# Kernel tuning notes

Hardware: AMD Instinct MI355X
Metric: run time of the kernel (lower is better)

## Reference

```python
import jax, jax.numpy as jnp
import numpy as np

IN_CHANNELS = 512
NUM_HEADS = 8
PARTIAL = 4
PC = IN_CHANNELS // PARTIAL  # 128, per-branch dim


def _mha(x, wqkv, bqkv, wproj, bproj, num_heads):
    # Standard ViT-style attention block: fused qkv -> SDPA -> out proj.
    B, N, C = x.shape
    d = C // num_heads
    qkv = (x @ wqkv + bqkv).reshape(B, N, 3, num_heads, d)
    q, k, v = jnp.moveaxis(qkv, 2, 0)            # each (B, N, h, d)
    q = q.transpose(0, 2, 1, 3)                  # (B, h, N, d)
    k = k.transpose(0, 2, 1, 3)
    v = v.transpose(0, 2, 1, 3)
    scale = jnp.asarray(d, x.dtype) ** -0.5
    attn = jax.nn.softmax(jnp.einsum('bhqd,bhkd->bhqk', q, k) * scale, axis=-1)
    out = jnp.einsum('bhqk,bhkd->bhqd', attn, v)
    out = out.transpose(0, 2, 1, 3).reshape(B, N, C)
    return out @ wproj + bproj


def _channel_shuffle(x, groups):
    # ShuffleNet channel shuffle on (b, c, n, t)
    b, c, n, t = x.shape
    return x.reshape(b, groups, c // groups, n, t).transpose(0, 2, 1, 3, 4).reshape(b, c, n, t)


def setup_inputs() -> dict:
    key = jax.random.key(0)
    ks = jax.random.split(key, 13)
    b, n, t = 8, 25, 64
    inp = {'x': jax.random.normal(ks[0], (b, n, t, IN_CHANNELS), dtype=jnp.float32)}
    i = 1
    for name in ('t', 's', 'st'):
        inp[f'{name}_wqkv'] = jax.random.normal(ks[i], (PC, 3 * PC), dtype=jnp.float32) * 0.02; i += 1
        inp[f'{name}_bqkv'] = jnp.zeros((3 * PC,), dtype=jnp.float32)
        inp[f'{name}_wproj'] = jax.random.normal(ks[i], (PC, PC), dtype=jnp.float32) * 0.02; i += 1
        inp[f'{name}_bproj'] = jnp.zeros((PC,), dtype=jnp.float32)
    return inp


def reference(x, t_wqkv, t_bqkv, t_wproj, t_bproj,
              s_wqkv, s_bqkv, s_wproj, s_bproj,
              st_wqkv, st_bqkv, st_wproj, st_bproj):
    b, n, t, c = x.shape
    pc = PC
    # split order in forward: x_id, x_st, x_s, x_t (all width pc here)
    x_id = x[..., 0 * pc:1 * pc]
    x_st = x[..., 1 * pc:2 * pc]
    x_s = x[..., 2 * pc:3 * pc]
    x_t = x[..., 3 * pc:4 * pc]

    t_x = x_t.reshape(b * n, t, pc)                       # temporal: attend over t
    s_x = x_s.transpose(0, 2, 1, 3).reshape(b * t, n, pc)  # spatial: attend over n
    st_x = x_st.reshape(b, n * t, pc)                      # spatiotemporal: attend over n*t

    t_x = _mha(t_x, t_wqkv, t_bqkv, t_wproj, t_bproj, NUM_HEADS).reshape(b, n, t, pc)
    s_x = _mha(s_x, s_wqkv, s_bqkv, s_wproj, s_bproj, NUM_HEADS).reshape(b, t, n, pc).transpose(0, 2, 1, 3)
    st_x = _mha(st_x, st_wqkv, st_bqkv, st_wproj, st_bproj, NUM_HEADS).reshape(b, n, t, pc)

    # concat order: id, t, s, st (differs from split order), then to channels-first
    out = jnp.concatenate((x_id, t_x, s_x, st_x), axis=3).transpose(0, 3, 1, 2)  # (b, c, n, t)
    return _channel_shuffle(out, PARTIAL)
```

## Files before the change

### kernel.cpp

```cpp
#include <hip/hip_runtime.h>
#include <hip/hip_bf16.h>

#define BUF   1638400ull
#define QSC   0.36067376f

typedef __attribute__((ext_vector_type(4))) float f4;
typedef __attribute__((ext_vector_type(8))) short s8v;
typedef __attribute__((ext_vector_type(4))) unsigned u4v;

#if __has_builtin(__builtin_amdgcn_exp2f)
#define EXP2(x) __builtin_amdgcn_exp2f(x)
#else
#define EXP2(x) exp2f(x)
#endif

__device__ __forceinline__ short f2bf(float f) {
    __hip_bfloat16 h = __float2bfloat16(f);
    short s; __builtin_memcpy(&s, &h, 2); return s;
}
__device__ __forceinline__ unsigned pack2(float a, float b) {
    return (unsigned)(unsigned short)f2bf(a) | ((unsigned)(unsigned short)f2bf(b) << 16);
}
__device__ __forceinline__ float bf2f(short s) {
    return __uint_as_float((unsigned)(unsigned short)s << 16);
}
__device__ __forceinline__ unsigned tpack(float hi, float lo) {
    return __builtin_amdgcn_perm(__float_as_uint(hi), __float_as_uint(lo), 0x07060302u);
}

__global__ __launch_bounds__(256) void prep(
    const float* __restrict__ x,
    const float* __restrict__ wq0, const float* __restrict__ wq1,
    const float* __restrict__ wq2,
    const float* __restrict__ wp0, const float* __restrict__ wp1,
    const float* __restrict__ wp2,
    short* __restrict__ xbf, short* __restrict__ wsw)
{
    const int blk = blockIdx.x, tid = threadIdx.x;
    if (blk < 3200) {
        const int base = blk * 2048 + tid * 8;
        float4 a = *(const float4*)(x + base);
        float4 b = *(const float4*)(x + base + 4);
        s8v o;
        o[0]=f2bf(a.x); o[1]=f2bf(a.y); o[2]=f2bf(a.z); o[3]=f2bf(a.w);
        o[4]=f2bf(b.x); o[5]=f2bf(b.y); o[6]=f2bf(b.z); o[7]=f2bf(b.w);
        *(s8v*)(xbf + base) = o;
    } else {
        const int idx0 = (blk - 3200) * 2048 + tid * 8;
        const float* W; int Ncols, loc = idx0;
        if      (idx0 < 49152)  { W = wq0; Ncols = 384; }
        else if (idx0 < 98304)  { W = wq1; Ncols = 384; loc -= 49152; }
        else if (idx0 < 147456) { W = wq2; Ncols = 384; loc -= 98304; }
        else if (idx0 < 163840) { W = wp0; Ncols = 128; loc -= 147456; }
        else if (idx0 < 180224) { W = wp1; Ncols = 128; loc -= 163840; }
        else                    { W = wp2; Ncols = 128; loc -= 180224; }
        const int lane = (loc >> 3) & 63, ks = (loc >> 9) & 3, nt = loc >> 11;
        const int col = nt * 16 + (lane & 15);
        const int k0  = ks * 32 + 8 * (lane >> 4);
        s8v o;
#pragma unroll
        for (int j = 0; j < 8; j++) o[j] = f2bf(W[(k0 + j) * Ncols + col]);
        *(s8v*)(wsw + idx0) = o;
    }
}

__global__ __launch_bounds__(256) void qkv_all(
    const short* __restrict__ xbf, const short* __restrict__ wsw,
    const float* __restrict__ bq0, const float* __restrict__ bq1,
    const float* __restrict__ bq2,
    short* __restrict__ q0, short* __restrict__ k0, short* __restrict__ vt0,
    short* __restrict__ q1, short* __restrict__ k1, short* __restrict__ vt1,
    short* __restrict__ q2, short* __restrict__ k2, short* __restrict__ vt2)
{
    const int br = blockIdx.x / 800, tile = blockIdx.x % 800;
    const int tok0 = tile * 16;
    const int wave = threadIdx.x >> 6, lane = threadIdx.x & 63;
    const int c = lane & 15, gq = lane >> 4;
    const int off = 384 - 128 * br;
    const short* wswb = wsw + br * 49152;
    const float* bias = (br == 0) ? bq0 : (br == 1) ? bq1 : bq2;

    const short* xrow = xbf + (size_t)(tok0 + c) * 512 + off + 8 * gq;
    s8v af[4];
#pragma unroll
    for (int ks = 0; ks < 4; ks++) af[ks] = *(const s8v*)(xrow + ks * 32);

    const int batch0 = tok0 >> 6;
    const int b_  = tok0 / 1600;
    const int rm0 = tok0 - b_ * 1600;
    const int seq1 = rm0 >> 6;

    for (int nti = 0; nti < 6; nti++) {
        const int nt = wave * 6 + nti;
        const short* bp = wswb + ((size_t)(nt * 4) * 64 + lane) * 8;
        f4 acc = {0.f, 0.f, 0.f, 0.f};
#pragma unroll
        for (int ks = 0; ks < 4; ks++) {
            s8v bf = *(const s8v*)(bp + ks * 512);
            acc = __builtin_amdgcn_mfma_f32_16x16x32_bf16(af[ks], bf, acc, 0, 0, 0);
        }
        const float bv = bias[nt * 16 + c];
        const float v0 = acc[0]+bv, v1 = acc[1]+bv, v2 = acc[2]+bv, v3 = acc[3]+bv;
        const int which = nt >> 3, h = nt & 7;

        if (br == 0) {
            const int seq0 = (tok0 & 63) + 4 * gq;
            if (which == 2) {
                unsigned* p = (unsigned*)(vt0 + ((size_t)(batch0*8+h)*16 + c)*64 + seq0);
                p[0] = pack2(v0, v1); p[1] = pack2(v2, v3);
            } else {
                short* p = (which ? k0 : q0) + (((size_t)(batch0*8+h)*64 + seq0)*16 + c);
                p[0]=f2bf(v0); p[16]=f2bf(v1); p[32]=f2bf(v2); p[48]=f2bf(v3);
            }
        } else if (br == 1) {
            const int bt0 = b_ * 64 + (rm0 & 63) + 4 * gq;
            if (which == 2) {
                short* p = vt1 + ((size_t)(bt0*8+h)*16 + c)*25 + seq1;
                p[0]=f2bf(v0); p[3200]=f2bf(v1); p[6400]=f2bf(v2); p[9600]=f2bf(v3);
            } else {
                short* p = (which ? k1 : q1) + (((size_t)bt0*8+h)*25 + seq1)*16 + c;
                p[0]=f2bf(v0); p[3200]=f2bf(v1); p[6400]=f2bf(v2); p[9600]=f2bf(v3);
            }
        } else {
            const int seq0 = rm0 + 4 * gq;
            if (which == 2) {
                unsigned* p = (unsigned*)(vt2 + ((size_t)b_*128 + h*16 + c)*1600 + seq0);
                p[0] = pack2(v0, v1); p[1] = pack2(v2, v3);
            } else {
                short* p = (which ? k2 : q2) + (((size_t)b_*8+h)*1600 + seq0)*16 + c;
                p[0]=f2bf(v0); p[16]=f2bf(v1); p[32]=f2bf(v2); p[48]=f2bf(v3);
            }
        }
    }
}

template<int CHK, int NCH, bool KM>
__device__ __forceinline__ void attn_core(
    const short* __restrict__ qg, const short* __restrict__ kg,
    const short* __restrict__ vtg, const int vstride, const int nreal,
    short* kl, short* vt, const int stid, const int snum,
    const int lane, const int qt0, const int nq,
    float* __restrict__ obase, const int ostride)
{
    const int c = lane & 15, gq = lane >> 4;
    const int VS = CHK + 8;

    u4v qu = {0u, 0u, 0u, 0u};
    if (gq < 2) {
        const int qrow = KM ? min(qt0 + c, nq - 1) : (qt0 + c);
        const short* qr = qg + (size_t)qrow * 16 + 8 * gq;
        s8v raw = *(const s8v*)qr;
#pragma unroll
        for (int jp = 0; jp < 4; jp++)
            qu[jp] = tpack(bf2f(raw[2*jp+1]) * QSC, bf2f(raw[2*jp]) * QSC);
    }
    const s8v qf = __builtin_bit_cast(s8v, qu);

    s8v ones;
#pragma unroll
    for (int j = 0; j < 8; j++) ones[j] = (short)0x3F80;

    f4 oacc = {0.f,0.f,0.f,0.f}, lacc = {0.f,0.f,0.f,0.f};
    const int krow_base = 8 * (c >> 2) + (c & 3);

    for (int ch = 0; ch < NCH; ch++) {
        const int kb0 = ch * CHK;
        __syncthreads();
        if (KM) {
            for (int i = stid; i < CHK * 16 + 8; i += snum)
                kl[i] = (i < nreal * 16) ? kg[i] : (short)0;
            for (int i = stid; i < 16 * VS; i += snum) {
                int d = i / VS, col = i % VS;
                vt[i] = (col < nreal) ? vtg[(size_t)d * vstride + col] : (short)0;
            }
        } else {
            const unsigned* kgd = (const unsigned*)(kg + (size_t)kb0 * 16);
            unsigned* kld = (unsigned*)kl;
            for (int i = stid; i < CHK * 8 + 4; i += snum)
                kld[i] = (i < CHK * 8) ? kgd[i] : 0u;
            for (int i = stid; i < 16 * (CHK / 2); i += snum) {
                int d = i / (CHK / 2), cc = i % (CHK / 2);
                *(unsigned*)(vt + d * VS + 2 * cc) =
                    *(const unsigned*)(vtg + (size_t)d * vstride + kb0 + 2 * cc);
            }
        }
        __syncthreads();

#pragma unroll
        for (int st = 0; st < CHK / 32; st++) {
            const int kr0 = st * 32 + krow_base;
            s8v kf0 = *(const s8v*)(gq < 2 ? kl + kr0 * 16 + 8 * gq       : kl + CHK * 16);
            s8v kf1 = *(const s8v*)(gq < 2 ? kl + (kr0 + 4) * 16 + 8 * gq : kl + CHK * 16);
            s8v vf  = *(const s8v*)(vt + c * VS + st * 32 + 8 * gq);

            const f4 z = {0.f,0.f,0.f,0.f};
            f4 sa = __builtin_amdgcn_mfma_f32_16x16x32_bf16(kf0, qf, z, 0, 0, 0);
            f4 sb = __builtin_amdgcn_mfma_f32_16x16x32_bf16(kf1, qf, z, 0, 0, 0);

            float pa[4], pb[4];
#pragma unroll
            for (int r = 0; r < 4; r++) { pa[r] = EXP2(sa[r]); pb[r] = EXP2(sb[r]); }
            if (KM) {
#pragma unroll
                for (int r = 0; r < 4; r++) {
                    if (kb0 + st*32 + 8*gq + r     >= nreal) pa[r] = 0.f;
                    if (kb0 + st*32 + 8*gq + 4 + r >= nreal) pb[r] = 0.f;
                }
            }
            u4v pu;
            pu[0] = tpack(pa[1], pa[0]); pu[1] = tpack(pa[3], pa[2]);
            pu[2] = tpack(pb[1], pb[0]); pu[3] = tpack(pb[3], pb[2]);
            s8v pf = __builtin_bit_cast(s8v, pu);

            oacc = __builtin_amdgcn_mfma_f32_16x16x32_bf16(pf, vf,   oacc, 0, 0, 0);
            lacc = __builtin_amdgcn_mfma_f32_16x16x32_bf16(pf, ones, lacc, 0, 0, 0);
        }
    }

#pragma unroll
    for (int r = 0; r < 4; r++) {
        const int qrow = qt0 + 4 * gq + r;
        if (!KM || qrow < nq)
            obase[(size_t)qrow * ostride] = oacc[r] / lacc[r];
    }
}

__global__ __launch_bounds__(256) void attn_all(
    const short* __restrict__ q0, const short* __restrict__ k0, const short* __restrict__ vt0,
    const short* __restrict__ q1, const short* __restrict__ k1, const short* __restrict__ vt1,
    const short* __restrict__ q2, const short* __restrict__ k2, const short* __restrict__ vt2,
    float* __restrict__ ob0, float* __restrict__ ob1, float* __restrict__ ob2)
{
    __shared__ short smem[5264];
    const int blk = blockIdx.x, tid = threadIdx.x;
    const int wave = tid >> 6, lane = tid & 63;
    const int c = lane & 15;

    if (blk < 1600) {
        const int bh = blk / 25, b25 = blk % 25;
        const int qt0 = b25 * 64 + wave * 16;
        float* obase = ob2 + (size_t)(bh >> 3) * 1600 * 128 + (bh & 7) * 16 + c;
        attn_core<160, 10, false>(q2 + (size_t)bh * 25600, k2 + (size_t)bh * 25600,
                                  vt2 + (size_t)bh * 25600, 1600, 1600,
                                  smem, smem + 2568, tid, 256,
                                  lane, qt0, 1600, obase, 128);
    } else if (blk < 3200) {
        const int bh = blk - 1600;
        float* obase = ob0 + (size_t)(bh >> 3) * 64 * 128 + (bh & 7) * 16 + c;
        attn_core<64, 1, false>(q0 + (size_t)bh * 1024, k0 + (size_t)bh * 1024,
                                vt0 + (size_t)bh * 1024, 64, 64,
                                smem, smem + 1040, tid, 256,
                                lane, wave * 16, 64, obase, 128);
    } else {
        const int bs = blk - 3200;
        const int half = wave >> 1;
        const int bh = bs * 2 + half;
        const int qt0 = (wave & 1) * 16;
        short* kl = smem + half * 1160;
        const int bat = bh >> 3, h = bh & 7;
        const int b2 = bat >> 6, t2 = bat & 63;
        float* obase = ob1 + ((size_t)b2 * 1600 + t2) * 128 + h * 16 + c;
        attn_core<32, 1, true>(q1 + (size_t)bh * 400, k1 + (size_t)bh * 400,
                               vt1 + (size_t)bh * 400, 25, 25,
                               kl, kl + 520, tid & 127, 128,
                               lane, qt0, 25, obase, 8192);
    }
}

__global__ __launch_bounds__(256) void projid(
    const float* __restrict__ ob0, const float* __restrict__ ob1,
    const float* __restrict__ ob2, const short* __restrict__ wsw,
    const float* __restrict__ bp0, const float* __restrict__ bp1,
    const float* __restrict__ bp2,
    const float* __restrict__ x, float* __restrict__ out)
{
    __shared__ unsigned short xl[64 * 130];
    const int blk = blockIdx.x, tid = threadIdx.x;

    if (blk < 2400) {
        const int br = blk / 800, t8 = blk % 800;
        const float* obb = (br == 0) ? ob0 : (br == 1) ? ob1 : ob2;
        const float* bp  = (br == 0) ? bp0 : (br == 1) ? bp1 : bp2;
        const short* wswb = wsw + 147456 + br * 16384;
        const int grp = br + 1;
        const int tok0 = t8 * 16;
        const int wave = tid >> 6, lane = tid & 63;
        const int c = lane & 15, gq = lane >> 4;

        const float* arow = obb + (size_t)(tok0 + c) * 128 + 8 * gq;
        s8v af[4];
#pragma unroll
        for (int ks = 0; ks < 4; ks++) {
            float4 a = *(const float4*)(arow + ks * 32);
            float4 b = *(const float4*)(arow + ks * 32 + 4);
            af[ks][0]=f2bf(a.x); af[ks][1]=f2bf(a.y); af[ks][2]=f2bf(a.z); af[ks][3]=f2bf(a.w);
            af[ks][4]=f2bf(b.x); af[ks][5]=f2bf(b.y); af[ks][6]=f2bf(b.z); af[ks][7]=f2bf(b.w);
        }

        const int bn = t8 >> 2, b_ = bn / 25, n_ = bn % 25;
        const int t0 = (t8 & 3) * 16 + 4 * gq;

        for (int nti = 0; nti < 2; nti++) {
            const int nt = wave * 2 + nti;
            const short* bpw = wswb + ((size_t)(nt * 4) * 64 + lane) * 8;
            f4 acc = {0.f, 0.f, 0.f, 0.f};
#pragma unroll
            for (int ks = 0; ks < 4; ks++) {
                s8v bf = *(const s8v*)(bpw + ks * 512);
                acc = __builtin_amdgcn_mfma_f32_16x16x32_bf16(af[ks], bf, acc, 0, 0, 0);
            }
            const int c2 = nt * 16 + c;
            const float bv = bp[c2];
            float4 st = {acc[0]+bv, acc[1]+bv, acc[2]+bv, acc[3]+bv};
            *(float4*)(out + (size_t)b_ * 819200 + (size_t)(c2 * 4 + grp) * 1600
                           + n_ * 64 + t0) = st;
        }
    } else {
        const int bn = blk - 2400;
        const int b_ = bn / 25, n_ = bn % 25;
        for (int idx = tid; idx < 8192; idx += 256) {
            int row = idx >> 7, c2 = idx & 127;
            xl[row * 130 + c2] =
                (unsigned short)(__float_as_uint(x[(size_t)(bn * 64 + row) * 512 + c2]) >> 16);
        }
        __syncthreads();
        const int t_ = tid & 63, cg = tid >> 6;
        const size_t base = (size_t)b_ * 819200 + (size_t)n_ * 64 + t_;
#pragma unroll
        for (int i = 0; i < 32; i++) {
            int c2 = cg + 4 * i;
            out[base + (size_t)(c2 * 4 + 0) * 1600] =
                __uint_as_float((unsigned)xl[t_ * 130 + c2] << 16);
        }
    }
}

extern "C" void kernel_launch(void* const* d_in, const int* in_sizes, int n_in,
                              void* d_out, int out_size, void* d_ws, size_t ws_size,
                              hipStream_t stream)
{
    const float* x        = (const float*)d_in[0];
    const float* t_wqkv   = (const float*)d_in[1];
    const float* t_bqkv   = (const float*)d_in[2];
    const float* t_wproj  = (const float*)d_in[3];
    const float* t_bproj  = (const float*)d_in[4];
    const float* s_wqkv   = (const float*)d_in[5];
    const float* s_bqkv   = (const float*)d_in[6];
    const float* s_wproj  = (const float*)d_in[7];
    const float* s_bproj  = (const float*)d_in[8];
    const float* st_wqkv  = (const float*)d_in[9];
    const float* st_bqkv  = (const float*)d_in[10];
    const float* st_wproj = (const float*)d_in[11];
    const float* st_bproj = (const float*)d_in[12];

    short* xbf = (short*)d_ws;
    short* wsw = xbf + 6553600ull;
    short* qkv = wsw + 196608ull;
    short *q0 = qkv,           *k0 = qkv + BUF,     *vt0 = qkv + 2*BUF;
    short *q1 = qkv + 3*BUF,   *k1 = qkv + 4*BUF,   *vt1 = qkv + 5*BUF;
    short *q2 = qkv + 6*BUF,   *k2 = qkv + 7*BUF,   *vt2 = qkv + 8*BUF;
    float* ob0 = (float*)(qkv + 9*BUF);
    float* ob1 = ob0 + BUF;
    float* ob2 = ob0 + 2*BUF;
    float* out = (float*)d_out;

    prep<<<3296, 256, 0, stream>>>(x, t_wqkv, s_wqkv, st_wqkv,
                                   t_wproj, s_wproj, st_wproj, xbf, wsw);
    qkv_all<<<2400, 256, 0, stream>>>(xbf, wsw, t_bqkv, s_bqkv, st_bqkv,
                                      q0, k0, vt0, q1, k1, vt1, q2, k2, vt2);
    attn_all<<<5248, 256, 0, stream>>>(q0, k0, vt0, q1, k1, vt1, q2, k2, vt2,
                                       ob0, ob1, ob2);
    projid<<<2600, 256, 0, stream>>>(ob0, ob1, ob2, wsw,
                                     t_bproj, s_bproj, st_bproj, x, out);
}
```

Baseline: 189.1 us.

## Rewrite attention with 32x32 MFMA, drop x bf16 prep pass, bf16 attention outputs

Removes the separate pass that converted x to bf16; the qkv kernel now reads fp32 x and packs it to bf16 inline. Attention moves from the LDS-staged 16x16 MFMA scheme to a per-wave 32x32x16 MFMA kernel that reads K/V directly from global memory with no shared memory or barriers. The softmax denominator comes from a row of ones in a global buffer fused into the PV MFMA and is read back with a lane shuffle. The spatial V buffer is padded to 32 and the attention outputs are written as bf16, which halves traffic into the projection kernel. The trade-offs are uncached global K/V loads and extra rounding of the intermediate outputs.

```diff
diff --git a/kernel.cpp b/kernel.cpp
--- a/kernel.cpp
+++ b/kernel.cpp
@@ -4,15 +4,21 @@
 #define BUF   1638400ull
 #define QSC   0.36067376f
 
-typedef __attribute__((ext_vector_type(4))) float f4;
-typedef __attribute__((ext_vector_type(8))) short s8v;
-typedef __attribute__((ext_vector_type(4))) unsigned u4v;
+typedef __attribute__((ext_vector_type(4)))  float    f4;
+typedef __attribute__((ext_vector_type(16))) float    f16v;
+typedef __attribute__((ext_vector_type(8)))  short    s8v;
+typedef __attribute__((ext_vector_type(4)))  unsigned u4v;
 
 #if __has_builtin(__builtin_amdgcn_exp2f)
 #define EXP2(x) __builtin_amdgcn_exp2f(x)
 #else
 #define EXP2(x) exp2f(x)
 #endif
+#if __has_builtin(__builtin_amdgcn_rcpf)
+#define RCP(x) __builtin_amdgcn_rcpf(x)
+#else
+#define RCP(x) (1.0f/(x))
+#endif
 
 __device__ __forceinline__ short f2bf(float f) {
     __hip_bfloat16 h = __float2bfloat16(f);
@@ -27,26 +33,23 @@
 __device__ __forceinline__ unsigned tpack(float hi, float lo) {
     return __builtin_amdgcn_perm(__float_as_uint(hi), __float_as_uint(lo), 0x07060302u);
 }
+__device__ __forceinline__ f16v zf16() {
+    f16v z;
+#pragma unroll
+    for (int i = 0; i < 16; i++) z[i] = 0.f;
+    return z;
+}
 
 __global__ __launch_bounds__(256) void prep(
-    const float* __restrict__ x,
     const float* __restrict__ wq0, const float* __restrict__ wq1,
     const float* __restrict__ wq2,
     const float* __restrict__ wp0, const float* __restrict__ wp1,
     const float* __restrict__ wp2,
-    short* __restrict__ xbf, short* __restrict__ wsw)
+    short* __restrict__ wsw, short* __restrict__ onesb)
 {
     const int blk = blockIdx.x, tid = threadIdx.x;
-    if (blk < 3200) {
-        const int base = blk * 2048 + tid * 8;
-        float4 a = *(const float4*)(x + base);
-        float4 b = *(const float4*)(x + base + 4);
-        s8v o;
-        o[0]=f2bf(a.x); o[1]=f2bf(a.y); o[2]=f2bf(a.z); o[3]=f2bf(a.w);
-        o[4]=f2bf(b.x); o[5]=f2bf(b.y); o[6]=f2bf(b.z); o[7]=f2bf(b.w);
-        *(s8v*)(xbf + base) = o;
-    } else {
-        const int idx0 = (blk - 3200) * 2048 + tid * 8;
+    if (blk < 96) {
+        const int idx0 = blk * 2048 + tid * 8;
         const float* W; int Ncols, loc = idx0;
         if      (idx0 < 49152)  { W = wq0; Ncols = 384; }
         else if (idx0 < 98304)  { W = wq1; Ncols = 384; loc -= 49152; }
@@ -61,11 +64,16 @@
 #pragma unroll
         for (int j = 0; j < 8; j++) o[j] = f2bf(W[(k0 + j) * Ncols + col]);
         *(s8v*)(wsw + idx0) = o;
+    } else {
+        s8v o;
+#pragma unroll
+        for (int j = 0; j < 8; j++) o[j] = (short)0x3F80;
+        *(s8v*)(onesb + tid * 8) = o;
     }
 }
 
 __global__ __launch_bounds__(256) void qkv_all(
-    const short* __restrict__ xbf, const short* __restrict__ wsw,
+    const float* __restrict__ x, const short* __restrict__ wsw,
     const float* __restrict__ bq0, const float* __restrict__ bq1,
     const float* __restrict__ bq2,
     short* __restrict__ q0, short* __restrict__ k0, short* __restrict__ vt0,
@@ -80,10 +88,17 @@
     const short* wswb = wsw + br * 49152;
     const float* bias = (br == 0) ? bq0 : (br == 1) ? bq1 : bq2;
 
-    const short* xrow = xbf + (size_t)(tok0 + c) * 512 + off + 8 * gq;
+    const float* xrow = x + (size_t)(tok0 + c) * 512 + off + 8 * gq;
     s8v af[4];
 #pragma unroll
-    for (int ks = 0; ks < 4; ks++) af[ks] = *(const s8v*)(xrow + ks * 32);
+    for (int ks = 0; ks < 4; ks++) {
+        float4 a = *(const float4*)(xrow + ks * 32);
+        float4 b = *(const float4*)(xrow + ks * 32 + 4);
+        u4v t;
+        t[0] = tpack(a.y, a.x); t[1] = tpack(a.w, a.z);
+        t[2] = tpack(b.y, b.x); t[3] = tpack(b.w, b.z);
+        af[ks] = __builtin_bit_cast(s8v, t);
+    }
 
     const int batch0 = tok0 >> 6;
     const int b_  = tok0 / 1600;
@@ -115,8 +130,8 @@
         } else if (br == 1) {
             const int bt0 = b_ * 64 + (rm0 & 63) + 4 * gq;
             if (which == 2) {
-                short* p = vt1 + ((size_t)(bt0*8+h)*16 + c)*25 + seq1;
-                p[0]=f2bf(v0); p[3200]=f2bf(v1); p[6400]=f2bf(v2); p[9600]=f2bf(v3);
+                short* p = vt1 + ((size_t)(bt0*8+h)*16 + c)*32 + seq1;
+                p[0]=f2bf(v0); p[4096]=f2bf(v1); p[8192]=f2bf(v2); p[12288]=f2bf(v3);
             } else {
                 short* p = (which ? k1 : q1) + (((size_t)bt0*8+h)*25 + seq1)*16 + c;
                 p[0]=f2bf(v0); p[3200]=f2bf(v1); p[6400]=f2bf(v2); p[9600]=f2bf(v3);
@@ -134,94 +149,63 @@
     }
 }
 
-template<int CHK, int NCH, bool KM>
-__device__ __forceinline__ void attn_core(
+template<int NSTEPS, bool MASK>
+__device__ __forceinline__ void attn32(
     const short* __restrict__ qg, const short* __restrict__ kg,
-    const short* __restrict__ vtg, const int vstride, const int nreal,
-    short* kl, short* vt, const int stid, const int snum,
-    const int lane, const int qt0, const int nq,
-    float* __restrict__ obase, const int ostride)
-{
-    const int c = lane & 15, gq = lane >> 4;
-    const int VS = CHK + 8;
-
-    u4v qu = {0u, 0u, 0u, 0u};
-    if (gq < 2) {
-        const int qrow = KM ? min(qt0 + c, nq - 1) : (qt0 + c);
-        const short* qr = qg + (size_t)qrow * 16 + 8 * gq;
-        s8v raw = *(const s8v*)qr;
-#pragma unroll
-        for (int jp = 0; jp < 4; jp++)
-            qu[jp] = tpack(bf2f(raw[2*jp+1]) * QSC, bf2f(raw[2*jp]) * QSC);
-    }
+    const short* __restrict__ vtg, const int vstride,
+    const short* __restrict__ onesb,
+    const int lane, const int qt0,
+    short* __restrict__ obase, const int orowstride, const int nq)
+{
+    const int n = lane & 31, g2 = lane >> 5;
+
+    s8v qraw = *(const s8v*)(qg + (size_t)(qt0 + n) * 16 + 8 * g2);
+    u4v qu;
+#pragma unroll
+    for (int jp = 0; jp < 4; jp++)
+        qu[jp] = tpack(bf2f(qraw[2*jp+1]) * QSC, bf2f(qraw[2*jp]) * QSC);
     const s8v qf = __builtin_bit_cast(s8v, qu);
 
-    s8v ones;
-#pragma unroll
-    for (int j = 0; j < 8; j++) ones[j] = (short)0x3F80;
-
-    f4 oacc = {0.f,0.f,0.f,0.f}, lacc = {0.f,0.f,0.f,0.f};
-    const int krow_base = 8 * (c >> 2) + (c & 3);
-
-    for (int ch = 0; ch < NCH; ch++) {
-        const int kb0 = ch * CHK;
-        __syncthreads();
-        if (KM) {
-            for (int i = stid; i < CHK * 16 + 8; i += snum)
-                kl[i] = (i < nreal * 16) ? kg[i] : (short)0;
-            for (int i = stid; i < 16 * VS; i += snum) {
-                int d = i / VS, col = i % VS;
-                vt[i] = (col < nreal) ? vtg[(size_t)d * vstride + col] : (short)0;
-            }
-        } else {
-            const unsigned* kgd = (const unsigned*)(kg + (size_t)kb0 * 16);
-            unsigned* kld = (unsigned*)kl;
-            for (int i = stid; i < CHK * 8 + 4; i += snum)
-                kld[i] = (i < CHK * 8) ? kgd[i] : 0u;
-            for (int i = stid; i < 16 * (CHK / 2); i += snum) {
-                int d = i / (CHK / 2), cc = i % (CHK / 2);
-                *(unsigned*)(vt + d * VS + 2 * cc) =
-                    *(const unsigned*)(vtg + (size_t)d * vstride + kb0 + 2 * cc);
-            }
-        }
-        __syncthreads();
-
-#pragma unroll
-        for (int st = 0; st < CHK / 32; st++) {
-            const int kr0 = st * 32 + krow_base;
-            s8v kf0 = *(const s8v*)(gq < 2 ? kl + kr0 * 16 + 8 * gq       : kl + CHK * 16);
-            s8v kf1 = *(const s8v*)(gq < 2 ? kl + (kr0 + 4) * 16 + 8 * gq : kl + CHK * 16);
-            s8v vf  = *(const s8v*)(vt + c * VS + st * 32 + 8 * gq);
-
-            const f4 z = {0.f,0.f,0.f,0.f};
-            f4 sa = __builtin_amdgcn_mfma_f32_16x16x32_bf16(kf0, qf, z, 0, 0, 0);
-            f4 sb = __builtin_amdgcn_mfma_f32_16x16x32_bf16(kf1, qf, z, 0, 0, 0);
-
-            float pa[4], pb[4];
-#pragma unroll
-            for (int r = 0; r < 4; r++) { pa[r] = EXP2(sa[r]); pb[r] = EXP2(sb[r]); }
-            if (KM) {
-#pragma unroll
-                for (int r = 0; r < 4; r++) {
-                    if (kb0 + st*32 + 8*gq + r     >= nreal) pa[r] = 0.f;
-                    if (kb0 + st*32 + 8*gq + 4 + r >= nreal) pb[r] = 0.f;
-                }
-            }
-            u4v pu;
-            pu[0] = tpack(pa[1], pa[0]); pu[1] = tpack(pa[3], pa[2]);
-            pu[2] = tpack(pb[1], pb[0]); pu[3] = tpack(pb[3], pb[2]);
-            s8v pf = __builtin_bit_cast(s8v, pu);
-
-            oacc = __builtin_amdgcn_mfma_f32_16x16x32_bf16(pf, vf,   oacc, 0, 0, 0);
-            lacc = __builtin_amdgcn_mfma_f32_16x16x32_bf16(pf, ones, lacc, 0, 0, 0);
-        }
-    }
-
-#pragma unroll
-    for (int r = 0; r < 4; r++) {
-        const int qrow = qt0 + 4 * gq + r;
-        if (!KM || qrow < nq)
-            obase[(size_t)qrow * ostride] = oacc[r] / lacc[r];
+    const int b4 = n >> 2;
+    const int krow = ((b4 ^ (((b4 ^ (b4 >> 1)) & 1) * 3)) << 2) + (n & 3);
+    const short* kp = kg + (size_t)krow * 16 + 8 * g2;
+    const short* vp = (n < 16) ? (vtg + (size_t)n * vstride + 8 * g2)
+                               : (onesb + 8 * g2);
+
+    f16v oacc = zf16();
+
+    for (int s = 0; s < NSTEPS; s++) {
+        s8v kf  = *(const s8v*)kp;  kp += 512;
+        s8v vf1 = *(const s8v*)vp;
+        s8v vf2 = *(const s8v*)(vp + 16); vp += 32;
+
+        f16v sacc = __builtin_amdgcn_mfma_f32_32x32x16_bf16(kf, qf, zf16(), 0, 0, 0);
+
+        float p[16];
+#pragma unroll
+        for (int r = 0; r < 16; r++) {
+            p[r] = EXP2(sacc[r]);
+            if (MASK && r >= 9) { if (g2) p[r] = 0.f; }
+        }
+        u4v u1, u2;
+        u1[0]=tpack(p[1],p[0]);   u1[1]=tpack(p[3],p[2]);
+        u1[2]=tpack(p[5],p[4]);   u1[3]=tpack(p[7],p[6]);
+        u2[0]=tpack(p[9],p[8]);   u2[1]=tpack(p[11],p[10]);
+        u2[2]=tpack(p[13],p[12]); u2[3]=tpack(p[15],p[14]);
+        s8v pf1 = __builtin_bit_cast(s8v, u1);
+        s8v pf2 = __builtin_bit_cast(s8v, u2);
+
+        oacc = __builtin_amdgcn_mfma_f32_32x32x16_bf16(pf1, vf1, oacc, 0, 0, 0);
+        oacc = __builtin_amdgcn_mfma_f32_32x32x16_bf16(pf2, vf2, oacc, 0, 0, 0);
+    }
+
+#pragma unroll
+    for (int r = 0; r < 16; r++) {
+        float l = __shfl_xor(oacc[r], 16);
+        float o = oacc[r] * RCP(l);
+        const int q = qt0 + (r & 3) + 8 * (r >> 2) + 4 * g2;
+        if (n < 16 && q < nq)
+            obase[(size_t)q * orowstride + n] = f2bf(o);
     }
 }
 
@@ -229,47 +213,43 @@
     const short* __restrict__ q0, const short* __restrict__ k0, const short* __restrict__ vt0,
     const short* __restrict__ q1, const short* __restrict__ k1, const short* __restrict__ vt1,
     const short* __restrict__ q2, const short* __restrict__ k2, const short* __restrict__ vt2,
-    float* __restrict__ ob0, float* __restrict__ ob1, float* __restrict__ ob2)
-{
-    __shared__ short smem[5264];
-    const int blk = blockIdx.x, tid = threadIdx.x;
-    const int wave = tid >> 6, lane = tid & 63;
-    const int c = lane & 15;
-
-    if (blk < 1600) {
-        const int bh = blk / 25, b25 = blk % 25;
-        const int qt0 = b25 * 64 + wave * 16;
-        float* obase = ob2 + (size_t)(bh >> 3) * 1600 * 128 + (bh & 7) * 16 + c;
-        attn_core<160, 10, false>(q2 + (size_t)bh * 25600, k2 + (size_t)bh * 25600,
-                                  vt2 + (size_t)bh * 25600, 1600, 1600,
-                                  smem, smem + 2568, tid, 256,
-                                  lane, qt0, 1600, obase, 128);
-    } else if (blk < 3200) {
-        const int bh = blk - 1600;
-        float* obase = ob0 + (size_t)(bh >> 3) * 64 * 128 + (bh & 7) * 16 + c;
-        attn_core<64, 1, false>(q0 + (size_t)bh * 1024, k0 + (size_t)bh * 1024,
-                                vt0 + (size_t)bh * 1024, 64, 64,
-                                smem, smem + 1040, tid, 256,
-                                lane, wave * 16, 64, obase, 128);
+    const short* __restrict__ onesb,
+    short* __restrict__ ob0, short* __restrict__ ob1, short* __restrict__ ob2)
+{
+    const int wave = threadIdx.x >> 6, lane = threadIdx.x & 63;
+    const int wid = blockIdx.x * 4 + wave;
+
+    if (wid < 3200) {
+        const int bh = wid / 50, qt0 = (wid % 50) * 32;
+        const int batch = bh >> 3, h = bh & 7;
+        attn32<50, false>(q2 + (size_t)bh * 25600, k2 + (size_t)bh * 25600,
+                          vt2 + (size_t)batch * 204800 + (size_t)h * 16 * 1600, 1600,
+                          onesb, lane, qt0,
+                          ob2 + (size_t)batch * 204800 + h * 16, 128, 1600);
+    } else if (wid < 6400) {
+        const int w = wid - 3200;
+        const int bh = w >> 1, qt0 = (w & 1) * 32;
+        const int bn = bh >> 3, h = bh & 7;
+        attn32<2, false>(q0 + (size_t)bh * 1024, k0 + (size_t)bh * 1024,
+                         vt0 + (size_t)bh * 1024, 64,
+                         onesb, lane, qt0,
+                         ob0 + (size_t)bn * 8192 + h * 16, 128, 64);
     } else {
-        const int bs = blk - 3200;
-        const int half = wave >> 1;
-        const int bh = bs * 2 + half;
-        const int qt0 = (wave & 1) * 16;
-        short* kl = smem + half * 1160;
-        const int bat = bh >> 3, h = bh & 7;
-        const int b2 = bat >> 6, t2 = bat & 63;
-        float* obase = ob1 + ((size_t)b2 * 1600 + t2) * 128 + h * 16 + c;
-        attn_core<32, 1, true>(q1 + (size_t)bh * 400, k1 + (size_t)bh * 400,
-                               vt1 + (size_t)bh * 400, 25, 25,
-                               kl, kl + 520, tid & 127, 128,
-                               lane, qt0, 25, obase, 8192);
+        const int bh = wid - 6400;
+        if (bh < 4096) {
+            const int bt = bh >> 3, h = bh & 7;
+            const int b_ = bt >> 6, t_ = bt & 63;
+            attn32<1, true>(q1 + (size_t)bh * 400, k1 + (size_t)bh * 400,
+                            vt1 + (size_t)bh * 512, 32,
+                            onesb, lane, 0,
+                            ob1 + (size_t)b_ * 204800 + t_ * 128 + h * 16, 8192, 25);
+        }
     }
 }
 
 __global__ __launch_bounds__(256) void projid(
-    const float* __restrict__ ob0, const float* __restrict__ ob1,
-    const float* __restrict__ ob2, const short* __restrict__ wsw,
+    const short* __restrict__ ob0, const short* __restrict__ ob1,
+    const short* __restrict__ ob2, const short* __restrict__ wsw,
     const float* __restrict__ bp0, const float* __restrict__ bp1,
     const float* __restrict__ bp2,
     const float* __restrict__ x, float* __restrict__ out)
@@ -279,7 +259,7 @@
 
     if (blk < 2400) {
         const int br = blk / 800, t8 = blk % 800;
-        const float* obb = (br == 0) ? ob0 : (br == 1) ? ob1 : ob2;
+        const short* obb = (br == 0) ? ob0 : (br == 1) ? ob1 : ob2;
         const float* bp  = (br == 0) ? bp0 : (br == 1) ? bp1 : bp2;
         const short* wswb = wsw + 147456 + br * 16384;
         const int grp = br + 1;
@@ -287,17 +267,12 @@
         const int wave = tid >> 6, lane = tid & 63;
         const int c = lane & 15, gq = lane >> 4;
 
-        const float* arow = obb + (size_t)(tok0 + c) * 128 + 8 * gq;
         s8v af[4];
 #pragma unroll
-        for (int ks = 0; ks < 4; ks++) {
-            float4 a = *(const float4*)(arow + ks * 32);
-            float4 b = *(const float4*)(arow + ks * 32 + 4);
-            af[ks][0]=f2bf(a.x); af[ks][1]=f2bf(a.y); af[ks][2]=f2bf(a.z); af[ks][3]=f2bf(a.w);
-            af[ks][4]=f2bf(b.x); af[ks][5]=f2bf(b.y); af[ks][6]=f2bf(b.z); af[ks][7]=f2bf(b.w);
-        }
-
-        const int bn = t8 >> 2, b_ = bn / 25, n_ = bn % 25;
+        for (int ks = 0; ks < 4; ks++)
+            af[ks] = *(const s8v*)(obb + (size_t)(tok0 + c) * 128 + ks * 32 + 8 * gq);
+
+        const int bnn = t8 >> 2, b_ = bnn / 25, n_ = bnn % 25;
         const int t0 = (t8 & 3) * 16 + 4 * gq;
 
         for (int nti = 0; nti < 2; nti++) {
@@ -353,23 +328,28 @@
     const float* st_wproj = (const float*)d_in[11];
     const float* st_bproj = (const float*)d_in[12];
 
-    short* xbf = (short*)d_ws;
-    short* wsw = xbf + 6553600ull;
-    short* qkv = wsw + 196608ull;
-    short *q0 = qkv,           *k0 = qkv + BUF,     *vt0 = qkv + 2*BUF;
-    short *q1 = qkv + 3*BUF,   *k1 = qkv + 4*BUF,   *vt1 = qkv + 5*BUF;
-    short *q2 = qkv + 6*BUF,   *k2 = qkv + 7*BUF,   *vt2 = qkv + 8*BUF;
-    float* ob0 = (float*)(qkv + 9*BUF);
-    float* ob1 = ob0 + BUF;
-    float* ob2 = ob0 + 2*BUF;
+    short* wsw   = (short*)d_ws;
+    short* onesb = wsw + 196608ull;
+    short* q0  = onesb + 2048ull;
+    short* k0  = q0 + BUF;
+    short* vt0 = k0 + BUF;
+    short* q1  = vt0 + BUF;
+    short* k1  = q1 + BUF;
+    short* vt1 = k1 + BUF;
+    short* q2  = vt1 + 2097152ull;
+    short* k2  = q2 + BUF;
+    short* vt2 = k2 + BUF;
+    short* ob0 = vt2 + BUF;
+    short* ob1 = ob0 + BUF;
+    short* ob2 = ob1 + BUF;
     float* out = (float*)d_out;
 
-    prep<<<3296, 256, 0, stream>>>(x, t_wqkv, s_wqkv, st_wqkv,
-                                   t_wproj, s_wproj, st_wproj, xbf, wsw);
-    qkv_all<<<2400, 256, 0, stream>>>(xbf, wsw, t_bqkv, s_bqkv, st_bqkv,
+    prep<<<97, 256, 0, stream>>>(t_wqkv, s_wqkv, st_wqkv,
+                                 t_wproj, s_wproj, st_wproj, wsw, onesb);
+    qkv_all<<<2400, 256, 0, stream>>>(x, wsw, t_bqkv, s_bqkv, st_bqkv,
                                       q0, k0, vt0, q1, k1, vt1, q2, k2, vt2);
-    attn_all<<<5248, 256, 0, stream>>>(q0, k0, vt0, q1, k1, vt1, q2, k2, vt2,
-                                       ob0, ob1, ob2);
+    attn_all<<<2624, 256, 0, stream>>>(q0, k0, vt0, q1, k1, vt1, q2, k2, vt2,
+                                       onesb, ob0, ob1, ob2);
     projid<<<2600, 256, 0, stream>>>(ob0, ob1, ob2, wsw,
                                      t_bproj, s_bproj, st_bproj, x, out);
 }
```

Result: faster. 180.3 us (-4.7%).
